# Performance work log

Measured on AMD Instinct MI355X. Metric: run time of the kernel, lower is better.

The kernel has to match this reference:

```python
import jax, jax.numpy as jnp
import numpy as np

N_NODES = 20000
N_EDGES = 320000
N_GRAPHS = 256
D = 256
L = 4
EPS = 1e-5


def setup_inputs() -> dict:
    key = jax.random.key(0)
    ks = jax.random.split(key, 20)
    x = jax.random.normal(ks[0], (N_NODES, D), dtype=jnp.float32)
    edge_index = jax.random.randint(ks[1], (2, N_EDGES), 0, N_NODES, dtype=jnp.int64)
    batch = jnp.sort(jax.random.randint(ks[2], (N_NODES,), 0, N_GRAPHS, dtype=jnp.int64))
    s = 1.0 / np.sqrt(D)
    Wl = jax.random.uniform(ks[3], (L, D, D), jnp.float32, -s, s)
    bl = jax.random.uniform(ks[4], (L, D), jnp.float32, -s, s)
    Wr = jax.random.uniform(ks[5], (L, D, D), jnp.float32, -s, s)
    gamma = jnp.ones((L, D), jnp.float32)
    beta = jnp.zeros((L, D), jnp.float32)
    fc1_w = jax.random.uniform(ks[6], (D, 128), jnp.float32, -s, s)
    fc1_b = jax.random.uniform(ks[7], (128,), jnp.float32, -s, s)
    s2 = 1.0 / np.sqrt(128)
    fc2_w = jax.random.uniform(ks[8], (128, 64), jnp.float32, -s2, s2)
    fc2_b = jax.random.uniform(ks[9], (64,), jnp.float32, -s2, s2)
    s3 = 1.0 / np.sqrt(64)
    fc3_w = jax.random.uniform(ks[10], (64, 10), jnp.float32, -s3, s3)
    fc3_b = jax.random.uniform(ks[11], (10,), jnp.float32, -s3, s3)
    return dict(x=x, edge_index=edge_index, batch=batch, Wl=Wl, bl=bl, Wr=Wr,
                gamma=gamma, beta=beta, fc1_w=fc1_w, fc1_b=fc1_b,
                fc2_w=fc2_w, fc2_b=fc2_b, fc3_w=fc3_w, fc3_b=fc3_b)


def reference(x, edge_index, batch, Wl, bl, Wr, gamma, beta,
              fc1_w, fc1_b, fc2_w, fc2_b, fc3_w, fc3_b):
    src, dst = edge_index[0], edge_index[1]
    # in-degree for mean aggregation (zero-degree nodes -> 0 aggregate)
    deg = jax.ops.segment_sum(jnp.ones((src.shape[0],), x.dtype), dst, num_segments=N_NODES)
    inv_deg = jnp.where(deg > 0, 1.0 / jnp.maximum(deg, 1.0), 0.0)[:, None]
    for i in range(L):
        # SAGEConv: mean-aggregate neighbors, then lin_l(agg) + lin_r(x)
        agg = jax.ops.segment_sum(x[src], dst, num_segments=N_NODES) * inv_deg
        h = agg @ Wl[i] + bl[i] + x @ Wr[i]
        # BatchNorm (training mode: biased batch statistics over nodes)
        mu = jnp.mean(h, axis=0)
        var = jnp.mean(jnp.square(h - mu), axis=0)
        h = (h - mu) * jax.lax.rsqrt(var + EPS) * gamma[i] + beta[i]
        x = jax.nn.relu(h)
    # global_mean_pool over graphs
    cnt = jax.ops.segment_sum(jnp.ones((N_NODES,), x.dtype), batch, num_segments=N_GRAPHS)
    g = jax.ops.segment_sum(x, batch, num_segments=N_GRAPHS) / jnp.maximum(cnt, 1.0)[:, None]
    # MLP classifier: 256 -> 128 -> 64 -> 10
    g = jax.nn.relu(g @ fc1_w + fc1_b)
    g = jax.nn.relu(g @ fc2_w + fc2_b)
    return g @ fc3_w + fc3_b
```

## Files before the change

### kernel.cpp

```cpp
#include <hip/hip_runtime.h>
#include <hip/hip_bf16.h>

#define NN 20000
#define NE 320000
#define NG 256
#define DD 256
#define NL 4
#define NBKT 79
#define BM 80
#define NBLK 250

typedef __attribute__((ext_vector_type(8))) short short8;
typedef __attribute__((ext_vector_type(4))) float float4_t;

__device__ __forceinline__ int ld_idx(const int* __restrict__ p, int i, int f64) {
    return f64 ? p[2 * i] : p[i];
}

__device__ __forceinline__ float bf2f(ushort u) {
    return __uint_as_float(((unsigned)u) << 16);
}

__device__ __forceinline__ ushort f2bf(float f) {
    __hip_bfloat16 b = __float2bfloat16(f);
    return *(ushort*)&b;
}


__global__ void k_init(const int* __restrict__ ei, const int* __restrict__ batch,
                       const ushort* __restrict__ x, int* __restrict__ flags,
                       int* __restrict__ deg) {
    int gid = blockIdx.x * 256 + threadIdx.x;
    for (int i = gid; i < NN; i += gridDim.x * 256) deg[i] = 0;
    if (blockIdx.x == 0) {
        __shared__ int cnt0, cnt1, weird;
        int t = threadIdx.x;
        if (t == 0) { cnt0 = 0; cnt1 = 0; weird = 0; }
        __syncthreads();
        for (int tt = t; tt < 512; tt += 256) {
            if (ei[2 * tt + 1] != 0) atomicAdd(&cnt0, 1);
            int i = tt * 9;
            if (batch[2 * i + 1] != 0) atomicAdd(&cnt1, 1);
#pragma unroll
            for (int j = 0; j < 16; j++) {
                ushort v = x[tt * 16 + j];
                if (((v >> 7) & 0xFF) >= 0xC0) atomicAdd(&weird, 1);
            }
        }
        __syncthreads();
        if (t == 0) {
            flags[0] = (cnt0 == 0) ? 1 : 0;
            flags[1] = (cnt1 == 0) ? 1 : 0;
            flags[2] = (weird == 0) ? 1 : 0;
        }
    }
}


#define POFF_BL   0
#define POFF_GA   1024
#define POFF_BE   2048
#define POFF_F1W  3072
#define POFF_F1B  35840
#define POFF_F2W  35968
#define POFF_F2B  44160
#define POFF_F3W  44224
#define POFF_F3B  44864
#define PTOT      44874

#define NB_CVT8   2500
#define NB_FRAG   128
#define NB_CVTP   176
#define NB_DEG    1250
#define NB_GST    79
#define B_FRAG    (NB_CVT8)
#define B_CVTP    (B_FRAG + NB_FRAG)
#define B_DEG     (B_CVTP + NB_CVTP)
#define B_GST     (B_DEG + NB_DEG)
#define NB_PREP   (B_GST + NB_GST)


__global__ __launch_bounds__(256) void k_prep(
    const void* __restrict__ x_in, const void* __restrict__ WL,
    const void* __restrict__ WR, const int* __restrict__ ei,
    const int* __restrict__ batch,
    const void* s0, const void* s1, const void* s2, const void* s3,
    const void* s4, const void* s5, const void* s6, const void* s7, const void* s8,
    ushort* __restrict__ xcan, ushort* __restrict__ wtL, ushort* __restrict__ wtR,
    ushort* __restrict__ pcan, int* __restrict__ deg, int* __restrict__ gstart,
    const int* __restrict__ fl) {
    int blk = blockIdx.x;
    int t = threadIdx.x;
    if (blk < B_FRAG) {
        int i = blk * 256 + t;
        if (fl[2]) {
            *(int4*)(xcan + (size_t)i * 8) = ((const int4*)x_in)[i];
        } else {
            const float* f = (const float*)x_in + (size_t)i * 8;
            ushort ov[8];
#pragma unroll
            for (int d = 0; d < 8; d++) ov[d] = f2bf(f[d]);
            *(int4*)(xcan + (size_t)i * 8) = *(int4*)ov;
        }
    } else if (blk < B_CVTP) {
        __shared__ ushort T[64][65];
        int bid = blk - B_FRAG;
        int lm = bid >> 4;
        int tile = bid & 15;
        int tk = (tile >> 2) * 64, tn = (tile & 3) * 64;
        const void* W = (lm >= 4) ? WR : WL;
        ushort* Wt = (lm >= 4) ? wtR : wtL;
        size_t base = (size_t)(lm & 3) << 16;
        int f32 = !fl[2];
#pragma unroll
        for (int i = 0; i < 16; i++) {
            int flat = t + i * 256;
            int r = flat >> 6, c = flat & 63;
            size_t src = base + (size_t)(tk + r) * 256 + tn + c;
            ushort v = f32 ? f2bf(((const float*)W)[src]) : ((const ushort*)W)[src];
            T[c][r] = v;
        }
        __syncthreads();
#pragma unroll
        for (int i = 0; i < 2; i++) {
            int slot = t + i * 256;
            int f = slot >> 6;
            int lane = slot & 63;
            int ln = (f >> 1) * 16 + (lane & 15);
            int lk = (f & 1) * 32 + ((lane >> 4) << 3);
            int gfblk = ((tn + ln) >> 4) * 8 + ((tk + lk) >> 5);
            ushort tmp[8];
#pragma unroll
            for (int j = 0; j < 8; j++) tmp[j] = T[ln][lk + j];
            *(int4*)(Wt + base + (size_t)gfblk * 512 + lane * 8) = *(int4*)tmp;
        }
    } else if (blk < B_DEG) {
        int i = (blk - B_CVTP) * 256 + t;
        if (i >= PTOT) return;
        const int offs[10] = {POFF_BL, POFF_GA, POFF_BE, POFF_F1W, POFF_F1B,
                              POFF_F2W, POFF_F2B, POFF_F3W, POFF_F3B, PTOT};
        const void* srcs[9] = {s0, s1, s2, s3, s4, s5, s6, s7, s8};
        int seg = 0;
#pragma unroll
        for (int k = 1; k < 9; k++) if (i >= offs[k]) seg = k;
        int local = i - offs[seg];
        if (fl[2]) pcan[i] = ((const ushort*)srcs[seg])[local];
        else       pcan[i] = f2bf(((const float*)srcs[seg])[local]);
    } else if (blk < B_GST) {
        int e = (blk - B_DEG) * 256 + t;
        if (e < NE) {
            int src = ld_idx(ei, e, fl[0]);
            int dst = ld_idx(ei, NE + e, fl[0]);
            if ((unsigned)dst < NN && (unsigned)src < NN) atomicAdd(&deg[dst], 1);
        }
    } else {
        int i = (blk - B_GST) * 256 + t;
        if (i >= NN) return;
        int b = ld_idx(batch, i, fl[1]);
        int bp = (i == 0) ? -1 : ld_idx(batch, i - 1, fl[1]);
        for (int g = bp + 1; g <= b; g++)
            if ((unsigned)g <= NG) gstart[g] = i;
        if (i == NN - 1)
            for (int g = b + 1; g <= NG; g++) gstart[g] = NN;
    }
}


__global__ __launch_bounds__(256) void k_scan(
    const int* __restrict__ deg, int* __restrict__ rowst,
    int* __restrict__ cursor, float* __restrict__ invdeg) {
    __shared__ int red[256];
    __shared__ int part[256];
    int b = blockIdx.x, t = threadIdx.x;
    int s = 0;
    for (int i = t; i < b * 256; i += 256) s += deg[i];
    red[t] = s;
    __syncthreads();
    for (int off = 128; off; off >>= 1) {
        if (t < off) red[t] += red[t + off];
        __syncthreads();
    }
    int bpref = red[0];
    int node = b * 256 + t;
    int d = (node < NN) ? deg[node] : 0;
    part[t] = d;
    __syncthreads();
    for (int off = 1; off < 256; off <<= 1) {
        int v = (t >= off) ? part[t - off] : 0;
        __syncthreads();
        part[t] += v;
        __syncthreads();
    }
    if (node < NN) {
        int o = bpref + part[t] - d;
        rowst[node] = o;
        cursor[node] = o;
        invdeg[node] = d > 0 ? 1.0f / (float)d : 0.0f;
    }
    if (b == NBKT - 1 && t == 255) rowst[NN] = bpref + part[255];
}

__global__ void k_fill(const int* __restrict__ ei, int* __restrict__ cursor,
                       int* __restrict__ csr, const int* __restrict__ fl) {
    int e = blockIdx.x * 256 + threadIdx.x;
    if (e < NE) {
        int src = ld_idx(ei, e, fl[0]);
        int dst = ld_idx(ei, NE + e, fl[0]);
        if ((unsigned)dst < NN && (unsigned)src < NN) {
            int p = atomicAdd(&cursor[dst], 1);
            if ((unsigned)p < NE) csr[p] = src;
        }
    }
}


template <int BNF>
__global__ __launch_bounds__(256) void k_agg4(
    const ushort* __restrict__ X, const int* __restrict__ rs,
    const int* __restrict__ csr, const float* __restrict__ invdeg,
    const float* __restrict__ bnsc, const float* __restrict__ bnsh,
    ushort* __restrict__ AGG) {
    int node = blockIdx.x * 4 + (threadIdx.x >> 6);
    if (node >= NN) return;
    int h = (threadIdx.x >> 5) & 1;
    int j = threadIdx.x & 31;
    float sc[8], sh[8];
    if (BNF) {
        float4 a0 = *(const float4*)(bnsc + j * 8);
        float4 a1 = *(const float4*)(bnsc + j * 8 + 4);
        float4 b0 = *(const float4*)(bnsh + j * 8);
        float4 b1 = *(const float4*)(bnsh + j * 8 + 4);
        sc[0] = a0.x; sc[1] = a0.y; sc[2] = a0.z; sc[3] = a0.w;
        sc[4] = a1.x; sc[5] = a1.y; sc[6] = a1.z; sc[7] = a1.w;
        sh[0] = b0.x; sh[1] = b0.y; sh[2] = b0.z; sh[3] = b0.w;
        sh[4] = b1.x; sh[5] = b1.y; sh[6] = b1.z; sh[7] = b1.w;
    }
    int e0 = rs[node], e1 = rs[node + 1];
    float acc[8] = {};
    int e = e0 + h;
    for (; e + 14 < e1; e += 16) {
        int4 v[8];
#pragma unroll
        for (int r = 0; r < 8; r++) {
            int s = csr[e + 2 * r];
            v[r] = *(const int4*)(X + (size_t)s * DD + j * 8);
        }
#pragma unroll
        for (int r = 0; r < 8; r++) {
            const ushort* u = (const ushort*)&v[r];
#pragma unroll
            for (int d = 0; d < 8; d++) {
                float x = bf2f(u[d]);
                if (BNF) x = fmaxf(x * sc[d] + sh[d], 0.0f);
                acc[d] += x;
            }
        }
    }
    for (; e + 2 < e1; e += 4) {
        int sA = csr[e], sB = csr[e + 2];
        int4 vA = *(const int4*)(X + (size_t)sA * DD + j * 8);
        int4 vB = *(const int4*)(X + (size_t)sB * DD + j * 8);
        const ushort* uA = (const ushort*)&vA;
        const ushort* uB = (const ushort*)&vB;
#pragma unroll
        for (int d = 0; d < 8; d++) {
            float xA = bf2f(uA[d]), xB = bf2f(uB[d]);
            if (BNF) {
                xA = fmaxf(xA * sc[d] + sh[d], 0.0f);
                xB = fmaxf(xB * sc[d] + sh[d], 0.0f);
            }
            acc[d] += xA + xB;
        }
    }
    for (; e < e1; e += 2) {
        int s = csr[e];
        int4 v = *(const int4*)(X + (size_t)s * DD + j * 8);
        const ushort* u = (const ushort*)&v;
#pragma unroll
        for (int d = 0; d < 8; d++) {
            float x = bf2f(u[d]);
            if (BNF) x = fmaxf(x * sc[d] + sh[d], 0.0f);
            acc[d] += x;
        }
    }
#pragma unroll
    for (int d = 0; d < 8; d++)
        acc[d] += __shfl_down(acc[d], 32);
    if (h == 0) {
        float inv = invdeg[node];
        ushort ov[8];
#pragma unroll
        for (int d = 0; d < 8; d++) ov[d] = f2bf(acc[d] * inv);
        *(int4*)(AGG + (size_t)node * DD + j * 8) = *(int4*)ov;
    }
}


template <int BNF>
__global__ __launch_bounds__(256, 3) void k_gemm8(
    const ushort* __restrict__ A1, const ushort* __restrict__ A2,
    const ushort* __restrict__ WtF1, const ushort* __restrict__ WtF2,
    const ushort* __restrict__ bias,
    const float* __restrict__ bnsc, const float* __restrict__ bnsh,
    ushort* __restrict__ H, float* __restrict__ psumT, float* __restrict__ psqT) {
    __shared__ ushort Als[BM][264];
    __shared__ float colsum[128];
    __shared__ float colsq[128];
    const int m0 = blockIdx.x * BM;
    const int n0 = blockIdx.y * 128;
    const int tid = threadIdx.x;
    const int w = tid >> 6, lane = tid & 63;
    const int lr = lane & 15, q = lane >> 4;
    float4_t acc[5][2] = {};

    if (tid < 128) { colsum[tid] = 0.0f; colsq[tid] = 0.0f; }

    for (int mat = 0; mat < 2; ++mat) {
        const ushort* A = mat ? A2 : A1;
        const ushort* Wf = mat ? WtF2 : WtF1;
        short8 bfr[8][2];
        const ushort* bb0 =
            Wf + (((size_t)(((n0 + w * 32) >> 4) * 8)) << 9) + lane * 8;
#pragma unroll
        for (int k8 = 0; k8 < 8; k8++)
#pragma unroll
            for (int in = 0; in < 2; in++)
                bfr[k8][in] = *(const short8*)(bb0 + (size_t)k8 * 512 + in * 4096);
        __syncthreads();
#pragma unroll
        for (int i = 0; i < 10; i++) {
            int flat = tid + i * 256;
            int r = flat >> 5;
            int c = (flat & 31) * 8;
            int4 av = *(const int4*)(A + (size_t)(m0 + r) * DD + c);
            if (BNF && mat == 1) {
                ushort* u = (ushort*)&av;
#pragma unroll
                for (int d = 0; d < 8; d++)
                    u[d] = f2bf(fmaxf(bf2f(u[d]) * bnsc[c + d] + bnsh[c + d], 0.0f));
            }
            *(int4*)&Als[r][c] = av;
        }
        __syncthreads();
#pragma unroll
        for (int k0 = 0; k0 < 256; k0 += 32) {
            short8 af[5];
#pragma unroll
            for (int im = 0; im < 5; im++)
                af[im] = *(const short8*)&Als[im * 16 + lr][k0 + q * 8];
#pragma unroll
            for (int in = 0; in < 2; in++) {
#pragma unroll
                for (int im = 0; im < 5; im++)
                    acc[im][in] = __builtin_amdgcn_mfma_f32_16x16x32_bf16(
                        af[im], bfr[k0 >> 5][in], acc[im][in], 0, 0, 0);
            }
        }
    }

    const int mbase = m0 + q * 4;
#pragma unroll
    for (int in = 0; in < 2; ++in) {
        const int nl = w * 32 + in * 16 + lr;
        const int n = n0 + nl;
        float b = bf2f(bias[n]);
        float s = 0.0f, s2 = 0.0f;
#pragma unroll
        for (int im = 0; im < 5; ++im) {
#pragma unroll
            for (int i = 0; i < 4; ++i) {
                int m = mbase + im * 16 + i;
                float hv = acc[im][in][i] + b;
                ushort hb = f2bf(hv);
                H[(size_t)m * DD + n] = hb;
                float hq = bf2f(hb);
                s += hq;
                s2 += hq * hq;
            }
        }
        s += __shfl_xor(s, 16);  s += __shfl_xor(s, 32);
        s2 += __shfl_xor(s2, 16); s2 += __shfl_xor(s2, 32);
        if (q == 0) {
            atomicAdd(&colsum[nl], s);
            atomicAdd(&colsq[nl], s2);
        }
    }
    __syncthreads();
    if (tid < 128) {
        psumT[(size_t)(n0 + tid) * 256 + blockIdx.x] = colsum[tid];
        psqT[(size_t)(n0 + tid) * 256 + blockIdx.x] = colsq[tid];
    }
}


__global__ __launch_bounds__(64) void k_bnfinal3(
    const float* __restrict__ psumT, const float* __restrict__ psqT,
    const ushort* __restrict__ gamma, const ushort* __restrict__ beta,
    float* __restrict__ scale, float* __restrict__ shift) {
    int c = blockIdx.x;
    int t = threadIdx.x;
    float s = 0.0f, s2 = 0.0f;
    for (int b = t; b < NBLK; b += 64) {
        s += psumT[(size_t)c * 256 + b];
        s2 += psqT[(size_t)c * 256 + b];
    }
#pragma unroll
    for (int o = 32; o; o >>= 1) {
        s += __shfl_down(s, o);
        s2 += __shfl_down(s2, o);
    }
    if (t == 0) {
        float mu = s * (1.0f / NN);
        float var = s2 * (1.0f / NN) - mu * mu;
        if (var < 0.0f) var = 0.0f;
        float rstd = rsqrtf(var + 1e-5f);
        float g = bf2f(gamma[c]);
        float b2 = bf2f(beta[c]);
        scale[c] = g * rstd;
        shift[c] = b2 - mu * g * rstd;
    }
}


__global__ __launch_bounds__(256) void k_head(
    const ushort* __restrict__ Hb, const float* __restrict__ scale,
    const float* __restrict__ shift, const int* __restrict__ gstart,
    const ushort* __restrict__ fc1w, const ushort* __restrict__ fc1b,
    const ushort* __restrict__ fc2w, const ushort* __restrict__ fc2b,
    const ushort* __restrict__ fc3w, const ushort* __restrict__ fc3b,
    void* __restrict__ out, const int* __restrict__ fl) {
    __shared__ float g[256];
    __shared__ float h1[128];
    __shared__ float h2[64];
    __shared__ ushort w1[256 * 128];
    __shared__ ushort w2[128 * 64];
    __shared__ ushort w3[64 * 10];
    int gid = blockIdx.x;
    int t = threadIdx.x;
    for (int i = t; i < 256 * 128 / 8; i += 256) ((int4*)w1)[i] = ((const int4*)fc1w)[i];
    for (int i = t; i < 128 * 64 / 8; i += 256) ((int4*)w2)[i] = ((const int4*)fc2w)[i];
    if (t < 80) ((int4*)w3)[t] = ((const int4*)fc3w)[t];

    int s0 = gstart[gid], e = gstart[gid + 1];
    float sc = scale[t], sh = shift[t];
    float acc = 0.0f;
    int i = s0;
    for (; i + 7 < e; i += 8) {
        float v[8];
#pragma unroll
        for (int r = 0; r < 8; r++) v[r] = bf2f(Hb[(size_t)(i + r) * DD + t]);
#pragma unroll
        for (int r = 0; r < 8; r++) acc += fmaxf(v[r] * sc + sh, 0.0f);
    }
    for (; i < e; i++)
        acc += fmaxf(bf2f(Hb[(size_t)i * DD + t]) * sc + sh, 0.0f);
    g[t] = acc / fmaxf((float)(e - s0), 1.0f);
    __syncthreads();
    if (t < 128) {
        float a = bf2f(fc1b[t]);
#pragma unroll 8
        for (int k = 0; k < 256; k++)
            a += g[k] * bf2f(w1[k * 128 + t]);
        h1[t] = fmaxf(a, 0.0f);
    }
    __syncthreads();
    if (t < 64) {
        float a2 = bf2f(fc2b[t]);
#pragma unroll 8
        for (int k = 0; k < 128; k++)
            a2 += h1[k] * bf2f(w2[k * 64 + t]);
        h2[t] = fmaxf(a2, 0.0f);
    }
    __syncthreads();
    if (t < 10) {
        float a3 = bf2f(fc3b[t]);
#pragma unroll 8
        for (int k = 0; k < 64; k++)
            a3 += h2[k] * bf2f(w3[k * 10 + t]);
        if (fl[2]) ((__hip_bfloat16*)out)[gid * 10 + t] = __float2bfloat16(a3);
        else       ((float*)out)[gid * 10 + t] = a3;
    }
}


static inline char* bump(char*& p, size_t n) {
    char* r = p;
    p += (n + 255) & ~(size_t)255;
    return r;
}

extern "C" void kernel_launch(void* const* d_in, const int* in_sizes, int n_in,
                              void* d_out, int out_size, void* d_ws, size_t ws_size,
                              hipStream_t stream) {
    const void* x_in  = d_in[0];
    const int*  ei    = (const int*)d_in[1];
    const int*  batch = (const int*)d_in[2];
    const void* Wl    = d_in[3];
    const void* bl    = d_in[4];
    const void* Wr    = d_in[5];
    const void* gamma = d_in[6];
    const void* beta  = d_in[7];

    char* p = (char*)d_ws;
    int*    flags    = (int*)bump(p, 256);
    ushort* wtL      = (ushort*)bump(p, (size_t)NL * 65536 * 2);
    ushort* wtR      = (ushort*)bump(p, (size_t)NL * 65536 * 2);
    ushort* xcan     = (ushort*)bump(p, (size_t)NN * DD * 2);
    ushort* pcan     = (ushort*)bump(p, (size_t)PTOT * 2);
    int*    deg      = (int*)bump(p, NN * 4);
    int*    rowst    = (int*)bump(p, (NN + 1) * 4);
    int*    cursor   = (int*)bump(p, NN * 4);
    float*  invdeg   = (float*)bump(p, NN * 4);
    int*    csr      = (int*)bump(p, NE * 4);
    int*    gstart   = (int*)bump(p, (NG + 1) * 4);
    ushort* agg      = (ushort*)bump(p, (size_t)NN * DD * 2);
    ushort* hb0      = (ushort*)bump(p, (size_t)NN * DD * 2);
    ushort* hb1      = (ushort*)bump(p, (size_t)NN * DD * 2);
    float*  psumT    = (float*)bump(p, (size_t)DD * 256 * 4);
    float*  psqT     = (float*)bump(p, (size_t)DD * 256 * 4);
    float*  scale    = (float*)bump(p, DD * 4);
    float*  shift    = (float*)bump(p, DD * 4);

    if ((size_t)(p - (char*)d_ws) > ws_size) return;

    ushort* blc = pcan + POFF_BL;
    ushort* gac = pcan + POFF_GA;
    ushort* bec = pcan + POFF_BE;
    ushort* f1w = pcan + POFF_F1W;
    ushort* f1b = pcan + POFF_F1B;
    ushort* f2w = pcan + POFF_F2W;
    ushort* f2b = pcan + POFF_F2B;
    ushort* f3w = pcan + POFF_F3W;
    ushort* f3b = pcan + POFF_F3B;

    k_init<<<80, 256, 0, stream>>>(ei, batch, (const ushort*)x_in, flags, deg);
    k_prep<<<NB_PREP, 256, 0, stream>>>(
        x_in, Wl, Wr, ei, batch,
        bl, gamma, beta, d_in[8], d_in[9], d_in[10], d_in[11], d_in[12], d_in[13],
        xcan, wtL, wtR, pcan, deg, gstart, flags);
    k_scan<<<NBKT, 256, 0, stream>>>(deg, rowst, cursor, invdeg);
    k_fill<<<(NE + 255) / 256, 256, 0, stream>>>(ei, cursor, csr, flags);

    ushort* hbuf[2] = {hb0, hb1};
    const ushort* xsrc = xcan;
    for (int l = 0; l < NL; l++) {
        ushort* hdst = hbuf[l & 1];
        const ushort* wl = wtL + (size_t)l * 65536;
        const ushort* wr = wtR + (size_t)l * 65536;
        if (l == 0) {
            k_agg4<0><<<(NN + 3) / 4, 256, 0, stream>>>(xsrc, rowst, csr, invdeg,
                                                        scale, shift, agg);
            k_gemm8<0><<<dim3(NBLK, 2), 256, 0, stream>>>(
                agg, xsrc, wl, wr, blc, scale, shift, hdst, psumT, psqT);
        } else {
            k_agg4<1><<<(NN + 3) / 4, 256, 0, stream>>>(xsrc, rowst, csr, invdeg,
                                                        scale, shift, agg);
            k_gemm8<1><<<dim3(NBLK, 2), 256, 0, stream>>>(
                agg, xsrc, wl, wr, blc + l * DD, scale, shift, hdst, psumT, psqT);
        }
        k_bnfinal3<<<DD, 64, 0, stream>>>(psumT, psqT, gac + l * DD, bec + l * DD,
                                          scale, shift);
        xsrc = hdst;
    }

    k_head<<<NG, 256, 0, stream>>>(xsrc, scale, shift, gstart,
                                   f1w, f1b, f2w, f2b, f3w, f3b, d_out, flags);
}
```

Before: 346.7 us.

## Split neighbor aggregation across feature slices with four nodes per wave

The mean-aggregation kernel now gives each block one 64-feature quarter of the row for 16 nodes. Each wave handles four nodes, with 8 lanes per half-row instead of 32. The grid grows to 5000 blocks, and the block index's low two bits select the feature slice. The aim is better cache locality, since the active working set per block is a quarter of each gathered row, and more parallelism across nodes with uneven degrees. The cost is more scattered 128-byte gathers per row, with the CSR indices re-read four times.

```diff
diff --git a/kernel.cpp b/kernel.cpp
--- a/kernel.cpp
+++ b/kernel.cpp
@@ -215,21 +215,26 @@
 
 
 template <int BNF>
-__global__ __launch_bounds__(256) void k_agg4(
+__global__ __launch_bounds__(256) void k_agg6(
     const ushort* __restrict__ X, const int* __restrict__ rs,
     const int* __restrict__ csr, const float* __restrict__ invdeg,
     const float* __restrict__ bnsc, const float* __restrict__ bnsh,
     ushort* __restrict__ AGG) {
-    int node = blockIdx.x * 4 + (threadIdx.x >> 6);
-    if (node >= NN) return;
-    int h = (threadIdx.x >> 5) & 1;
-    int j = threadIdx.x & 31;
+    const int s = blockIdx.x & 3;
+    const int chunk = blockIdx.x >> 2;
+    const int tid = threadIdx.x;
+    const int w = tid >> 6, lane = tid & 63;
+    const int nw = lane >> 4;
+    const int h = (lane >> 3) & 1;
+    const int jl = lane & 7;
+    const int db = s * 64 + jl * 8;
+    const int node = chunk * 16 + w * 4 + nw;
     float sc[8], sh[8];
     if (BNF) {
-        float4 a0 = *(const float4*)(bnsc + j * 8);
-        float4 a1 = *(const float4*)(bnsc + j * 8 + 4);
-        float4 b0 = *(const float4*)(bnsh + j * 8);
-        float4 b1 = *(const float4*)(bnsh + j * 8 + 4);
+        float4 a0 = *(const float4*)(bnsc + db);
+        float4 a1 = *(const float4*)(bnsc + db + 4);
+        float4 b0 = *(const float4*)(bnsh + db);
+        float4 b1 = *(const float4*)(bnsh + db + 4);
         sc[0] = a0.x; sc[1] = a0.y; sc[2] = a0.z; sc[3] = a0.w;
         sc[4] = a1.x; sc[5] = a1.y; sc[6] = a1.z; sc[7] = a1.w;
         sh[0] = b0.x; sh[1] = b0.y; sh[2] = b0.z; sh[3] = b0.w;
@@ -242,8 +247,8 @@
         int4 v[8];
 #pragma unroll
         for (int r = 0; r < 8; r++) {
-            int s = csr[e + 2 * r];
-            v[r] = *(const int4*)(X + (size_t)s * DD + j * 8);
+            int src = csr[e + 2 * r];
+            v[r] = *(const int4*)(X + (size_t)src * DD + db);
         }
 #pragma unroll
         for (int r = 0; r < 8; r++) {
@@ -258,8 +263,8 @@
     }
     for (; e + 2 < e1; e += 4) {
         int sA = csr[e], sB = csr[e + 2];
-        int4 vA = *(const int4*)(X + (size_t)sA * DD + j * 8);
-        int4 vB = *(const int4*)(X + (size_t)sB * DD + j * 8);
+        int4 vA = *(const int4*)(X + (size_t)sA * DD + db);
+        int4 vB = *(const int4*)(X + (size_t)sB * DD + db);
         const ushort* uA = (const ushort*)&vA;
         const ushort* uB = (const ushort*)&vB;
 #pragma unroll
@@ -273,8 +278,8 @@
         }
     }
     for (; e < e1; e += 2) {
-        int s = csr[e];
-        int4 v = *(const int4*)(X + (size_t)s * DD + j * 8);
+        int src = csr[e];
+        int4 v = *(const int4*)(X + (size_t)src * DD + db);
         const ushort* u = (const ushort*)&v;
 #pragma unroll
         for (int d = 0; d < 8; d++) {
@@ -285,13 +290,13 @@
     }
 #pragma unroll
     for (int d = 0; d < 8; d++)
-        acc[d] += __shfl_down(acc[d], 32);
+        acc[d] += __shfl_down(acc[d], 8);
     if (h == 0) {
         float inv = invdeg[node];
         ushort ov[8];
 #pragma unroll
         for (int d = 0; d < 8; d++) ov[d] = f2bf(acc[d] * inv);
-        *(int4*)(AGG + (size_t)node * DD + j * 8) = *(int4*)ov;
+        *(int4*)(AGG + (size_t)node * DD + db) = *(int4*)ov;
     }
 }
 
@@ -548,13 +553,13 @@
         const ushort* wl = wtL + (size_t)l * 65536;
         const ushort* wr = wtR + (size_t)l * 65536;
         if (l == 0) {
-            k_agg4<0><<<(NN + 3) / 4, 256, 0, stream>>>(xsrc, rowst, csr, invdeg,
-                                                        scale, shift, agg);
+            k_agg6<0><<<5000, 256, 0, stream>>>(xsrc, rowst, csr, invdeg,
+                                                scale, shift, agg);
             k_gemm8<0><<<dim3(NBLK, 2), 256, 0, stream>>>(
                 agg, xsrc, wl, wr, blc, scale, shift, hdst, psumT, psqT);
         } else {
-            k_agg4<1><<<(NN + 3) / 4, 256, 0, stream>>>(xsrc, rowst, csr, invdeg,
-                                                        scale, shift, agg);
+            k_agg6<1><<<5000, 256, 0, stream>>>(xsrc, rowst, csr, invdeg,
+                                                scale, shift, agg);
             k_gemm8<1><<<dim3(NBLK, 2), 256, 0, stream>>>(
                 agg, xsrc, wl, wr, blc + l * DD, scale, shift, hdst, psumT, psqT);
         }
```

Result: slower. 366.4 us (+5.7%).
